# Kernel tuning notes

Measured on AMD Instinct MI355X. Metric: run time of the kernel, lower is better.

Reference implementation:

```python
import jax, jax.numpy as jnp
import numpy as np

N, E, DIN, DOUT = 50000, 625000, 128, 128


def setup_inputs() -> dict:
    key = jax.random.key(0)
    k = jax.random.split(key, 4)
    x = jax.random.normal(k[0], (N, DIN), dtype=jnp.float32)
    edge_index = jax.random.randint(k[1], (2, E), 0, N, dtype=jnp.int32)
    s = 1.0 / np.sqrt(DIN)  # Glorot-ish init like torch Linear
    W_fwd = jax.random.uniform(k[2], (DIN, DOUT), jnp.float32, -s, s)
    W_bwd = jax.random.uniform(k[3], (DIN, DOUT), jnp.float32, -s, s)
    b_fwd = jnp.zeros((DOUT,), jnp.float32)
    b_bwd = jnp.zeros((DOUT,), jnp.float32)
    return {"x": x, "edge_index": edge_index, "W_fwd": W_fwd, "b_fwd": b_fwd,
            "W_bwd": W_bwd, "b_bwd": b_bwd}


def gcn_conv(x, W, b, src, dst, n):
    """PyG GCNConv: add self-loops, symmetric degree norm, gather-scatter aggregate."""
    loops = jnp.arange(n, dtype=src.dtype)
    src2 = jnp.concatenate([src, loops])  # [E+N]
    dst2 = jnp.concatenate([dst, loops])
    ones = jnp.ones(src2.shape[0], dtype=x.dtype)
    deg = jax.ops.segment_sum(ones, dst2, num_segments=n)  # in-degree incl. self-loop
    dinv = jnp.where(deg > 0, jax.lax.rsqrt(deg), 0.0)
    norm = dinv[src2] * dinv[dst2]  # [E+N]
    h = x @ W  # [N, DOUT] dense GEMM before message passing
    msgs = h[src2] * norm[:, None]  # gather + scale, [E+N, DOUT]
    out = jax.ops.segment_sum(msgs, dst2, num_segments=n)  # scatter-add
    return out + b


def reference(x, edge_index, W_fwd, b_fwd, W_bwd, b_bwd):
    src, dst = edge_index[0], edge_index[1]
    n = x.shape[0]
    x_forward = gcn_conv(x, W_fwd, b_fwd, src, dst, n)
    # reversed edge direction for the backward diffusion conv
    x_backward = gcn_conv(x, W_bwd, b_bwd, dst, src, n)
    # dropout omitted (eval mode / deterministic reference)
    return jax.nn.relu(x_forward + x_backward)
```

## Files before the change

### kernel.cpp

```cpp
#include <hip/hip_runtime.h>
#include <hip/hip_bf16.h>
#include <cstdint>

static constexpr int BLK      = 256;
static constexpr int CAP      = 40;
static constexpr int BINSHIFT = 8;
static constexpr int BINNODES = 1 << BINSHIFT;
static constexpr int BINCAP   = BINNODES * CAP / 2;
static constexpr int EPB      = 2048;
static constexpr int OVMAX    = 1024;
static constexpr int NB2MAX   = 512;

typedef __attribute__((ext_vector_type(8))) short bf16x8;
typedef __attribute__((ext_vector_type(4))) float f32x4;

__device__ __forceinline__ float bf16lo(uint32_t u) { return __uint_as_float(u << 16); }
__device__ __forceinline__ float bf16hi(uint32_t u) { return __uint_as_float(u & 0xffff0000u); }
__device__ __forceinline__ unsigned short f2bf(float f) {
    __hip_bfloat16 h = __float2bfloat16(f);
    return *(unsigned short*)&h;
}

__global__ __launch_bounds__(BLK) void k_bin(
        const int* __restrict__ src, const int* __restrict__ dst, int ne,
        uint32_t* __restrict__ pair, int* __restrict__ gcnt,
        int* __restrict__ ovcnt, int* __restrict__ ovlist, int nbins) {
    __shared__ uint32_t stage[EPB * 2];
    __shared__ int hist[NB2MAX];
    __shared__ int lofs[NB2MAX];
    __shared__ int gbase[NB2MAX];
    __shared__ int chunk[NB2MAX / 8];
    const int tid = threadIdx.x, bid = blockIdx.x;
    const int nb2 = 2 * nbins;
    for (int i = tid; i < nb2; i += BLK) hist[i] = 0;
    __syncthreads();

    int s[8], d[8];
    const int e0 = bid * EPB + tid;
#pragma unroll
    for (int k = 0; k < 8; ++k) {
        int e = e0 + k * BLK;
        bool v = e < ne;
        s[k] = v ? src[e] : -1;
        d[k] = v ? dst[e] : -1;
        if (v) {
            atomicAdd(&hist[d[k] >> BINSHIFT], 1);
            atomicAdd(&hist[nbins + (s[k] >> BINSHIFT)], 1);
        }
    }
    __syncthreads();

    const int nch = (nb2 + 7) >> 3;
    if (tid < nch) {
        int a = 0, base = tid << 3;
#pragma unroll
        for (int k = 0; k < 8; ++k) { int idx = base + k; if (idx < nb2) a += hist[idx]; }
        chunk[tid] = a;
    }
    __syncthreads();
    if (tid == 0) { int a = 0; for (int c = 0; c < nch; ++c) { int t = chunk[c]; chunk[c] = a; a += t; } }
    __syncthreads();
    for (int i = tid; i < nb2; i += BLK) {
        int a = chunk[i >> 3];
        for (int k = (i >> 3) << 3; k < i; ++k) a += hist[k];
        lofs[i] = a;
    }
    __syncthreads();
    for (int i = tid; i < nb2; i += BLK) {
        int c = hist[i];
        gbase[i] = c ? atomicAdd(&gcnt[i], c) : 0;
        hist[i] = lofs[i];
    }
    __syncthreads();
#pragma unroll
    for (int k = 0; k < 8; ++k) {
        if (s[k] >= 0) {
            int b0 = d[k] >> BINSHIFT;
            int p0 = atomicAdd(&hist[b0], 1);
            stage[p0] = ((uint32_t)d[k] << 16) | (uint32_t)s[k];
            int b1 = nbins + (s[k] >> BINSHIFT);
            int p1 = atomicAdd(&hist[b1], 1);
            stage[p1] = ((uint32_t)s[k] << 16) | (uint32_t)d[k];
        }
    }
    __syncthreads();
    int nval = ne - bid * EPB; if (nval > EPB) nval = EPB; if (nval < 0) nval = 0;
    const int total = 2 * nval;
    for (int i = tid; i < total; i += BLK) {
        int lo = 0, hi = nb2 - 1;
        while (lo < hi) { int mid = (lo + hi + 1) >> 1; if (lofs[mid] <= i) lo = mid; else hi = mid - 1; }
        int gidx = gbase[lo] + (i - lofs[lo]);
        if (gidx < BINCAP)
            pair[(size_t)lo * BINCAP + gidx] = stage[i];
        else {
            int node = (int)(stage[i] >> 16);
            int q = atomicAdd(ovcnt, 1);
            if (q < OVMAX) ovlist[q] = (node << 1) | (lo >= nbins ? 1 : 0);
        }
    }
}

__global__ __launch_bounds__(BLK) void k_build_conv(
        uint32_t* __restrict__ pair, const int* __restrict__ gcnt,
        int* __restrict__ cnt_f, int* __restrict__ cnt_b,
        float* __restrict__ dinv_f, float* __restrict__ dinv_b,
        int* __restrict__ ovcnt, int* __restrict__ ovlist,
        const float* __restrict__ x, uint32_t* __restrict__ xb32, int nxw, int gxc,
        const float* __restrict__ Wf, const float* __restrict__ Wb,
        unsigned short* __restrict__ WTf, unsigned short* __restrict__ WTb,
        int n, int nbins) {
    const int bid = blockIdx.x, tid = threadIdx.x;
    const int nb2 = 2 * nbins;
    if (bid < nb2) {
        __shared__ unsigned short buck[BINNODES * CAP];
        __shared__ int lcnt[BINNODES];
        lcnt[tid] = 0;
        __syncthreads();
        int count = gcnt[bid]; if (count > BINCAP) count = BINCAP;
        const uint32_t* pb = pair + (size_t)bid * BINCAP;
        const int dir = bid >= nbins ? 1 : 0;
        for (int i = tid; i < count; i += BLK) {
            uint32_t p = pb[i];
            int l = (p >> 16) & (BINNODES - 1);
            int r = atomicAdd(&lcnt[l], 1);
            if (r < CAP) buck[l * CAP + r] = (unsigned short)(p & 0xffffu);
            else {
                int q = atomicAdd(ovcnt, 1);
                if (q < OVMAX)
                    ovlist[q] = (((((bid - dir * nbins) << BINSHIFT) + l)) << 1) | dir;
            }
        }
        __syncthreads();
        const int node = ((bid - dir * nbins) << BINSHIFT) + tid;
        if (node < n) {
            int c = lcnt[tid];
            if (dir) { cnt_b[node] = c; dinv_b[node] = rsqrtf(1.0f + (float)c); }
            else     { cnt_f[node] = c; dinv_f[node] = rsqrtf(1.0f + (float)c); }
        }
        uint32_t* seg = pair + (size_t)bid * BINCAP;
        const uint32_t* b32 = (const uint32_t*)buck;
        for (int i = tid; i < BINCAP; i += BLK) seg[i] = b32[i];
        return;
    }
    if (bid < nb2 + gxc) {
        int base = (bid - nb2) * 2048;
        int end = base + 2048; if (end > nxw) end = nxw;
        for (int i = base + tid; i < end; i += BLK) {
            float2 v = ((const float2*)x)[i];
            xb32[i] = ((uint32_t)f2bf(v.y) << 16) | (uint32_t)f2bf(v.x);
        }
        return;
    }
    int wb = bid - nb2 - gxc;
    for (int idx = wb * 2048 + tid; idx < (wb + 1) * 2048; idx += BLK) {
        int c = idx >> 7, k = idx & 127;
        WTf[c * 128 + k] = f2bf(Wf[k * 128 + c]);
        WTb[c * 128 + k] = f2bf(Wb[k * 128 + c]);
    }
}

__device__ __forceinline__ void accum_range(
        int j0, int j1, int ofs, float sc,
        const uint32_t* __restrict__ xb, int lane, float& a0, float& a1) {
    int j = j0;
    for (; j + 8 <= j1; j += 8) {
        int   o0 = __shfl(ofs, j + 0), o1 = __shfl(ofs, j + 1);
        int   o2 = __shfl(ofs, j + 2), o3 = __shfl(ofs, j + 3);
        int   o4 = __shfl(ofs, j + 4), o5 = __shfl(ofs, j + 5);
        int   o6 = __shfl(ofs, j + 6), o7 = __shfl(ofs, j + 7);
        float s0 = __shfl(sc, j + 0), s1 = __shfl(sc, j + 1);
        float s2 = __shfl(sc, j + 2), s3 = __shfl(sc, j + 3);
        float s4 = __shfl(sc, j + 4), s5 = __shfl(sc, j + 5);
        float s6 = __shfl(sc, j + 6), s7 = __shfl(sc, j + 7);
        uint32_t u0 = xb[(size_t)(o0 + lane)], u1 = xb[(size_t)(o1 + lane)];
        uint32_t u2 = xb[(size_t)(o2 + lane)], u3 = xb[(size_t)(o3 + lane)];
        uint32_t u4 = xb[(size_t)(o4 + lane)], u5 = xb[(size_t)(o5 + lane)];
        uint32_t u6 = xb[(size_t)(o6 + lane)], u7 = xb[(size_t)(o7 + lane)];
        a0 = fmaf(s0, bf16lo(u0), a0); a1 = fmaf(s0, bf16hi(u0), a1);
        a0 = fmaf(s1, bf16lo(u1), a0); a1 = fmaf(s1, bf16hi(u1), a1);
        a0 = fmaf(s2, bf16lo(u2), a0); a1 = fmaf(s2, bf16hi(u2), a1);
        a0 = fmaf(s3, bf16lo(u3), a0); a1 = fmaf(s3, bf16hi(u3), a1);
        a0 = fmaf(s4, bf16lo(u4), a0); a1 = fmaf(s4, bf16hi(u4), a1);
        a0 = fmaf(s5, bf16lo(u5), a0); a1 = fmaf(s5, bf16hi(u5), a1);
        a0 = fmaf(s6, bf16lo(u6), a0); a1 = fmaf(s6, bf16hi(u6), a1);
        a0 = fmaf(s7, bf16lo(u7), a0); a1 = fmaf(s7, bf16hi(u7), a1);
    }
    for (; j + 4 <= j1; j += 4) {
        int   o0 = __shfl(ofs, j + 0), o1 = __shfl(ofs, j + 1);
        int   o2 = __shfl(ofs, j + 2), o3 = __shfl(ofs, j + 3);
        float s0 = __shfl(sc, j + 0), s1 = __shfl(sc, j + 1);
        float s2 = __shfl(sc, j + 2), s3 = __shfl(sc, j + 3);
        uint32_t u0 = xb[(size_t)(o0 + lane)], u1 = xb[(size_t)(o1 + lane)];
        uint32_t u2 = xb[(size_t)(o2 + lane)], u3 = xb[(size_t)(o3 + lane)];
        a0 = fmaf(s0, bf16lo(u0), a0); a1 = fmaf(s0, bf16hi(u0), a1);
        a0 = fmaf(s1, bf16lo(u1), a0); a1 = fmaf(s1, bf16hi(u1), a1);
        a0 = fmaf(s2, bf16lo(u2), a0); a1 = fmaf(s2, bf16hi(u2), a1);
        a0 = fmaf(s3, bf16lo(u3), a0); a1 = fmaf(s3, bf16hi(u3), a1);
    }
    for (; j < j1; ++j) {
        int oj = __shfl(ofs, j); float sj = __shfl(sc, j);
        uint32_t uj = xb[(size_t)(oj + lane)];
        a0 = fmaf(sj, bf16lo(uj), a0); a1 = fmaf(sj, bf16hi(uj), a1);
    }
}

__global__ __launch_bounds__(BLK) void k_gather_agg(
        const int* __restrict__ cnt_f, const int* __restrict__ cnt_b,
        const unsigned short* __restrict__ adj_f,
        const unsigned short* __restrict__ adj_b,
        const float* __restrict__ dinv_f, const float* __restrict__ dinv_b,
        const uint32_t* __restrict__ xb32,
        uint32_t* __restrict__ agg32,
        int n, int gnode,
        const int* __restrict__ ovcnt, const int* __restrict__ ovlist,
        const int* __restrict__ src, const int* __restrict__ dst, int ne) {
    const int bid = blockIdx.x;
    if (bid < gnode) {
        const int wave = threadIdx.x >> 6;
        const int lane = threadIdx.x & 63;
        const int node = bid * 4 + wave;
        if (node >= n) return;

        int cf = cnt_f[node], cb = cnt_b[node];
        if (cf > CAP || cb > CAP) return;

        float dvsf = dinv_f[node], dvsb = dinv_b[node];
        uint32_t uv = xb32[(size_t)node * 64 + lane];
        float accf0 = dvsf * dvsf * bf16lo(uv), accf1 = dvsf * dvsf * bf16hi(uv);
        float accb0 = dvsb * dvsb * bf16lo(uv), accb1 = dvsb * dvsb * bf16hi(uv);

        const int mt = cf + cb;
        if (mt <= 64) {
            int ofs = 0; float sc = 0.f;
            if (lane < cf) {
                int nb = adj_f[node * CAP + lane];
                ofs = nb * 64;
                sc  = dvsf * dinv_f[nb];
            } else if (lane < mt) {
                int nb = adj_b[node * CAP + (lane - cf)];
                ofs = nb * 64;
                sc  = dvsb * dinv_b[nb];
            }
            accum_range(0,  cf, ofs, sc, xb32, lane, accf0, accf1);
            accum_range(cf, mt, ofs, sc, xb32, lane, accb0, accb1);
        } else {
            for (int j = 0; j < cf; ++j) {
                int nb = adj_f[node * CAP + j];
                float dj = dvsf * dinv_f[nb];
                uint32_t u = xb32[(size_t)nb * 64 + lane];
                accf0 = fmaf(dj, bf16lo(u), accf0); accf1 = fmaf(dj, bf16hi(u), accf1);
            }
            for (int j = 0; j < cb; ++j) {
                int nb = adj_b[node * CAP + j];
                float dj = dvsb * dinv_b[nb];
                uint32_t u = xb32[(size_t)nb * 64 + lane];
                accb0 = fmaf(dj, bf16lo(u), accb0); accb1 = fmaf(dj, bf16hi(u), accb1);
            }
        }
        agg32[(size_t)node * 128 + lane] =
            ((uint32_t)f2bf(accf1) << 16) | (uint32_t)f2bf(accf0);
        agg32[(size_t)node * 128 + 64 + lane] =
            ((uint32_t)f2bf(accb1) << 16) | (uint32_t)f2bf(accb0);
        return;
    }

    int nov = *ovcnt; if (nov > OVMAX) nov = OVMAX;
    if (nov == 0) return;
    __shared__ int lst[4096];
    __shared__ int lc;
    const int tid = threadIdx.x;
    for (int i = bid - gnode; i < nov; i += 8) {
        int node = ovlist[i] >> 1;
        for (int d2 = 0; d2 < 2; ++d2) {
            const int* key = d2 ? src : dst;
            const int* val = d2 ? dst : src;
            const float* dinv = d2 ? dinv_b : dinv_f;
            float dvs = dinv[node];
            float s0 = 0.f, s1 = 0.f;
            if (tid < 64) {
                uint32_t u = xb32[(size_t)node * 64 + tid];
                s0 = dvs * bf16lo(u); s1 = dvs * bf16hi(u);
            }
            for (int start = 0; start < ne; start += 4096) {
                if (tid == 0) lc = 0;
                __syncthreads();
                int end = min(start + 4096, ne);
                for (int e2 = start + tid; e2 < end; e2 += BLK)
                    if (key[e2] == node) { int q = atomicAdd(&lc, 1); lst[q] = val[e2]; }
                __syncthreads();
                int mm = lc;
                if (tid < 64) {
                    for (int j = 0; j < mm; ++j) {
                        int nb = lst[j];
                        float dv = dinv[nb];
                        uint32_t u = xb32[(size_t)nb * 64 + tid];
                        s0 = fmaf(dv, bf16lo(u), s0);
                        s1 = fmaf(dv, bf16hi(u), s1);
                    }
                }
                __syncthreads();
            }
            if (tid < 64) {
                float a0 = dvs * s0, a1 = dvs * s1;
                agg32[(size_t)node * 128 + d2 * 64 + tid] =
                    ((uint32_t)f2bf(a1) << 16) | (uint32_t)f2bf(a0);
            }
            __syncthreads();
        }
    }
}

__global__ __launch_bounds__(BLK) void k_gemm_out(
        const unsigned short* __restrict__ agg,
        const unsigned short* __restrict__ WTf,
        const unsigned short* __restrict__ WTb,
        const float* __restrict__ bfv, const float* __restrict__ bbv,
        float* __restrict__ out, int n) {
    const int wave = threadIdx.x >> 6, lane = threadIdx.x & 63;
    const int wm = wave >> 1, wh = wave & 1;
    const int q = lane >> 4, t16 = lane & 15;
    const int m0 = blockIdx.x * 32 + wm * 16;
    int arow = m0 + t16; if (arow >= n) arow = n - 1;
    const unsigned short* ra = agg + (size_t)arow * 256;
    bf16x8 af[4], ab[4];
#pragma unroll
    for (int s = 0; s < 4; ++s) {
        af[s] = *(const bf16x8*)(ra + s * 32 + q * 8);
        ab[s] = *(const bf16x8*)(ra + 128 + s * 32 + q * 8);
    }
    __syncthreads();
#pragma unroll
    for (int t = 0; t < 4; ++t) {
        const int col = wh * 64 + t * 16 + t16;
        const unsigned short* wrf = WTf + (size_t)col * 128;
        const unsigned short* wrb = WTb + (size_t)col * 128;
        f32x4 c = {0.f, 0.f, 0.f, 0.f};
#pragma unroll
        for (int s = 0; s < 4; ++s)
            c = __builtin_amdgcn_mfma_f32_16x16x32_bf16(
                    af[s], *(const bf16x8*)(wrf + s * 32 + q * 8), c, 0, 0, 0);
#pragma unroll
        for (int s = 0; s < 4; ++s)
            c = __builtin_amdgcn_mfma_f32_16x16x32_bf16(
                    ab[s], *(const bf16x8*)(wrb + s * 32 + q * 8), c, 0, 0, 0);
        const float bias = bfv[col] + bbv[col];
#pragma unroll
        for (int r = 0; r < 4; ++r) {
            int row = m0 + q * 4 + r;
            if (row < n)
                out[(size_t)row * 128 + col] = fmaxf(c[r] + bias, 0.f);
        }
    }
}

extern "C" void kernel_launch(void* const* d_in, const int* in_sizes, int n_in,
                              void* d_out, int out_size, void* d_ws, size_t ws_size,
                              hipStream_t stream) {
    const float* x  = (const float*)d_in[0];
    const int*   ei = (const int*)d_in[1];
    const float* Wf = (const float*)d_in[2];
    const float* bf = (const float*)d_in[3];
    const float* Wb = (const float*)d_in[4];
    const float* bb = (const float*)d_in[5];

    const int n  = in_sizes[0] / 128;
    const int ne = in_sizes[1] / 2;
    const int* src = ei;
    const int* dst = ei + ne;
    float* out = (float*)d_out;

    const int nbins = (n + BINNODES - 1) >> BINSHIFT;
    const int nb2   = 2 * nbins;

    char* w = (char*)d_ws;
    uint32_t* pair = (uint32_t*)w;              w += (size_t)nb2 * BINCAP * 4;
    uint32_t* xb32 = (uint32_t*)w;              w += (size_t)n * 64 * 4;
    float* dinv_f = (float*)w;                  w += (size_t)n * 4;
    float* dinv_b = (float*)w;                  w += (size_t)n * 4;
    unsigned short* WTf = (unsigned short*)w;   w += 128 * 128 * 2;
    unsigned short* WTb = (unsigned short*)w;   w += 128 * 128 * 2;
    int* cnt_f = (int*)w;                       w += (size_t)n * 4;
    int* cnt_b = (int*)w;                       w += (size_t)n * 4;
    int* gcnt = (int*)w;                        w += (size_t)nb2 * 4;
    int* ovcnt = (int*)w;                       w += 8 * 4;
    int* ovlist = (int*)w;                      w += OVMAX * 4;

    const unsigned short* adj_f = (const unsigned short*)pair;
    const unsigned short* adj_b = adj_f + (size_t)nbins * BINNODES * CAP;
    uint32_t* agg32 = (uint32_t*)d_out;

    const int gbin  = (ne + EPB - 1) / EPB;
    const int gxc   = (n * 64 + 2047) / 2048;
    const int gnode = (n + 3) / 4;
    const int ggo   = (n + 31) / 32;

    hipMemsetAsync(gcnt, 0, (size_t)(nb2 + 8) * 4, stream);

    k_bin<<<gbin, BLK, 0, stream>>>(src, dst, ne, pair, gcnt, ovcnt, ovlist, nbins);

    k_build_conv<<<nb2 + gxc + 8, BLK, 0, stream>>>(pair, gcnt,
                                                    cnt_f, cnt_b, dinv_f, dinv_b,
                                                    ovcnt, ovlist,
                                                    x, xb32, n * 64, gxc,
                                                    Wf, Wb, WTf, WTb, n, nbins);

    k_gather_agg<<<gnode + 8, BLK, 0, stream>>>(cnt_f, cnt_b, adj_f, adj_b,
                                                dinv_f, dinv_b, xb32,
                                                agg32, n, gnode,
                                                ovcnt, ovlist, src, dst, ne);

    k_gemm_out<<<ggo, BLK, 0, stream>>>((const unsigned short*)agg32,
                                        WTf, WTb, bf, bb, out, n);
}
```

Measured before the change: 199.4 us.

## Fuse all phases into one persistent cooperative kernel with grid syncs

Replaces the memset and four separate kernel launches with a single cooperative persistent kernel. Its five phases (weight and x conversion, edge binning, bucket build, gather-aggregate, MFMA GEMM) are separated by grid-wide syncs and use grid-stride loops. It also halves edges per binning block and records each staged entry's bin index, so the per-element binary search is no longer needed. The aim is to remove launch gaps and the memset. In exchange, occupancy is capped by the cooperative grid size, and grid syncs plus grid-stride loops add overhead to the memory-bound gather phase.

After: 597.6 us. 3x slower.

```diff
diff --git a/kernel.cpp b/kernel.cpp
--- a/kernel.cpp
+++ b/kernel.cpp
@@ -1,15 +1,18 @@
 #include <hip/hip_runtime.h>
 #include <hip/hip_bf16.h>
+#include <hip/hip_cooperative_groups.h>
 #include <cstdint>
 
-static constexpr int BLK      = 256;
+namespace cg = cooperative_groups;
+
 static constexpr int CAP      = 40;
 static constexpr int BINSHIFT = 8;
 static constexpr int BINNODES = 1 << BINSHIFT;
 static constexpr int BINCAP   = BINNODES * CAP / 2;
-static constexpr int EPB      = 2048;
+static constexpr int EPB      = 1024;
 static constexpr int OVMAX    = 1024;
 static constexpr int NB2MAX   = 512;
+static constexpr int SMEM_SZ  = 21504;
 
 typedef __attribute__((ext_vector_type(8))) short bf16x8;
 typedef __attribute__((ext_vector_type(4))) float f32x4;
@@ -21,145 +24,157 @@
     return *(unsigned short*)&h;
 }
 
-__global__ __launch_bounds__(BLK) void k_bin(
-        const int* __restrict__ src, const int* __restrict__ dst, int ne,
-        uint32_t* __restrict__ pair, int* __restrict__ gcnt,
-        int* __restrict__ ovcnt, int* __restrict__ ovlist, int nbins) {
-    __shared__ uint32_t stage[EPB * 2];
-    __shared__ int hist[NB2MAX];
-    __shared__ int lofs[NB2MAX];
-    __shared__ int gbase[NB2MAX];
-    __shared__ int chunk[NB2MAX / 8];
-    const int tid = threadIdx.x, bid = blockIdx.x;
-    const int nb2 = 2 * nbins;
-    for (int i = tid; i < nb2; i += BLK) hist[i] = 0;
-    __syncthreads();
-
-    int s[8], d[8];
-    const int e0 = bid * EPB + tid;
-#pragma unroll
-    for (int k = 0; k < 8; ++k) {
-        int e = e0 + k * BLK;
-        bool v = e < ne;
-        s[k] = v ? src[e] : -1;
-        d[k] = v ? dst[e] : -1;
-        if (v) {
-            atomicAdd(&hist[d[k] >> BINSHIFT], 1);
-            atomicAdd(&hist[nbins + (s[k] >> BINSHIFT)], 1);
-        }
-    }
-    __syncthreads();
-
-    const int nch = (nb2 + 7) >> 3;
-    if (tid < nch) {
-        int a = 0, base = tid << 3;
-#pragma unroll
-        for (int k = 0; k < 8; ++k) { int idx = base + k; if (idx < nb2) a += hist[idx]; }
-        chunk[tid] = a;
-    }
-    __syncthreads();
-    if (tid == 0) { int a = 0; for (int c = 0; c < nch; ++c) { int t = chunk[c]; chunk[c] = a; a += t; } }
-    __syncthreads();
-    for (int i = tid; i < nb2; i += BLK) {
-        int a = chunk[i >> 3];
-        for (int k = (i >> 3) << 3; k < i; ++k) a += hist[k];
-        lofs[i] = a;
-    }
-    __syncthreads();
-    for (int i = tid; i < nb2; i += BLK) {
-        int c = hist[i];
-        gbase[i] = c ? atomicAdd(&gcnt[i], c) : 0;
-        hist[i] = lofs[i];
-    }
-    __syncthreads();
-#pragma unroll
-    for (int k = 0; k < 8; ++k) {
-        if (s[k] >= 0) {
-            int b0 = d[k] >> BINSHIFT;
-            int p0 = atomicAdd(&hist[b0], 1);
-            stage[p0] = ((uint32_t)d[k] << 16) | (uint32_t)s[k];
-            int b1 = nbins + (s[k] >> BINSHIFT);
-            int p1 = atomicAdd(&hist[b1], 1);
-            stage[p1] = ((uint32_t)s[k] << 16) | (uint32_t)d[k];
-        }
-    }
-    __syncthreads();
-    int nval = ne - bid * EPB; if (nval > EPB) nval = EPB; if (nval < 0) nval = 0;
-    const int total = 2 * nval;
-    for (int i = tid; i < total; i += BLK) {
-        int lo = 0, hi = nb2 - 1;
-        while (lo < hi) { int mid = (lo + hi + 1) >> 1; if (lofs[mid] <= i) lo = mid; else hi = mid - 1; }
-        int gidx = gbase[lo] + (i - lofs[lo]);
-        if (gidx < BINCAP)
-            pair[(size_t)lo * BINCAP + gidx] = stage[i];
-        else {
-            int node = (int)(stage[i] >> 16);
-            int q = atomicAdd(ovcnt, 1);
-            if (q < OVMAX) ovlist[q] = (node << 1) | (lo >= nbins ? 1 : 0);
-        }
-    }
-}
-
-__global__ __launch_bounds__(BLK) void k_build_conv(
-        uint32_t* __restrict__ pair, const int* __restrict__ gcnt,
-        int* __restrict__ cnt_f, int* __restrict__ cnt_b,
-        float* __restrict__ dinv_f, float* __restrict__ dinv_b,
-        int* __restrict__ ovcnt, int* __restrict__ ovlist,
-        const float* __restrict__ x, uint32_t* __restrict__ xb32, int nxw, int gxc,
-        const float* __restrict__ Wf, const float* __restrict__ Wb,
-        unsigned short* __restrict__ WTf, unsigned short* __restrict__ WTb,
-        int n, int nbins) {
-    const int bid = blockIdx.x, tid = threadIdx.x;
-    const int nb2 = 2 * nbins;
-    if (bid < nb2) {
-        __shared__ unsigned short buck[BINNODES * CAP];
-        __shared__ int lcnt[BINNODES];
+struct P {
+    const int* src; const int* dst; int ne;
+    uint32_t* pair; int* gcnt; int* ovcnt; int* ovlist;
+    int nbins, nb2, gbin, gxc, ggo, n;
+    const float* x; uint32_t* xb32; int nxw;
+    const float* Wf; const float* Wb;
+    unsigned short* WTf; unsigned short* WTb;
+    int* cnt_f; int* cnt_b; float* dinv_f; float* dinv_b;
+    const unsigned short* adj_f; const unsigned short* adj_b;
+    const float* bfv; const float* bbv;
+    float* out;
+};
+
+__device__ void phaseA(const P& A) {
+    const int G = gridDim.x, tid = threadIdx.x;
+    const int ta = 9 + A.gxc;
+    for (int t = blockIdx.x; t < ta; t += G) {
+        if (t < 8) {
+            for (int idx = t * 2048 + tid; idx < (t + 1) * 2048; idx += 256) {
+                int c = idx >> 7, k = idx & 127;
+                A.WTf[c * 128 + k] = f2bf(A.Wf[k * 128 + c]);
+                A.WTb[c * 128 + k] = f2bf(A.Wb[k * 128 + c]);
+            }
+        } else if (t == 8) {
+            for (int i = tid; i < A.nb2 + 8; i += 256) A.gcnt[i] = 0;
+        } else {
+            int base = (t - 9) * 2048;
+            int end = base + 2048; if (end > A.nxw) end = A.nxw;
+            for (int i = base + tid; i < end; i += 256) {
+                float2 v = ((const float2*)A.x)[i];
+                A.xb32[i] = ((uint32_t)f2bf(v.y) << 16) | (uint32_t)f2bf(v.x);
+            }
+        }
+    }
+}
+
+__device__ void phaseB(const P& A, char* smem) {
+    uint32_t*       stage = (uint32_t*)smem;
+    unsigned short* binof = (unsigned short*)(smem + 8192);
+    int*            hist  = (int*)(smem + 12288);
+    int*            lofs  = (int*)(smem + 14336);
+    int*            gbase = (int*)(smem + 16384);
+    int*            chunk = (int*)(smem + 18432);
+    const int G = gridDim.x, tid = threadIdx.x;
+    const int nb2 = A.nb2;
+    for (int t = blockIdx.x; t < A.gbin; t += G) {
+        for (int i = tid; i < nb2; i += 256) hist[i] = 0;
+        __syncthreads();
+        int s[4], d[4];
+        const int e0 = t * EPB + tid;
+#pragma unroll
+        for (int k = 0; k < 4; ++k) {
+            int e = e0 + k * 256;
+            bool v = e < A.ne;
+            s[k] = v ? A.src[e] : -1;
+            d[k] = v ? A.dst[e] : -1;
+            if (v) {
+                atomicAdd(&hist[d[k] >> BINSHIFT], 1);
+                atomicAdd(&hist[A.nbins + (s[k] >> BINSHIFT)], 1);
+            }
+        }
+        __syncthreads();
+        const int nch = (nb2 + 7) >> 3;
+        if (tid < nch) {
+            int a = 0, base = tid << 3;
+#pragma unroll
+            for (int k = 0; k < 8; ++k) { int idx = base + k; if (idx < nb2) a += hist[idx]; }
+            chunk[tid] = a;
+        }
+        __syncthreads();
+        if (tid == 0) { int a = 0; for (int c = 0; c < nch; ++c) { int tt = chunk[c]; chunk[c] = a; a += tt; } }
+        __syncthreads();
+        for (int i = tid; i < nb2; i += 256) {
+            int a = chunk[i >> 3];
+            for (int k = (i >> 3) << 3; k < i; ++k) a += hist[k];
+            lofs[i] = a;
+        }
+        __syncthreads();
+        for (int i = tid; i < nb2; i += 256) {
+            int c = hist[i];
+            gbase[i] = c ? atomicAdd(&A.gcnt[i], c) : 0;
+            hist[i] = lofs[i];
+        }
+        __syncthreads();
+#pragma unroll
+        for (int k = 0; k < 4; ++k) {
+            if (s[k] >= 0) {
+                int b0 = d[k] >> BINSHIFT;
+                int p0 = atomicAdd(&hist[b0], 1);
+                stage[p0] = ((uint32_t)d[k] << 16) | (uint32_t)s[k];
+                binof[p0] = (unsigned short)b0;
+                int b1 = A.nbins + (s[k] >> BINSHIFT);
+                int p1 = atomicAdd(&hist[b1], 1);
+                stage[p1] = ((uint32_t)s[k] << 16) | (uint32_t)d[k];
+                binof[p1] = (unsigned short)b1;
+            }
+        }
+        __syncthreads();
+        int nval = A.ne - t * EPB; if (nval > EPB) nval = EPB; if (nval < 0) nval = 0;
+        const int total = 2 * nval;
+        for (int i = tid; i < total; i += 256) {
+            int b = binof[i];
+            int gidx = gbase[b] + (i - lofs[b]);
+            if (gidx < BINCAP)
+                A.pair[(size_t)b * BINCAP + gidx] = stage[i];
+            else {
+                int node = (int)(stage[i] >> 16);
+                int q = atomicAdd(A.ovcnt, 1);
+                if (q < OVMAX) A.ovlist[q] = (node << 1) | (b >= A.nbins ? 1 : 0);
+            }
+        }
+        __syncthreads();
+    }
+}
+
+__device__ void phaseC(const P& A, char* smem) {
+    unsigned short* buck = (unsigned short*)smem;
+    int*            lcnt = (int*)(smem + 20480);
+    const int tid = threadIdx.x;
+    for (int b = blockIdx.x; b < A.nb2; b += gridDim.x) {
         lcnt[tid] = 0;
         __syncthreads();
-        int count = gcnt[bid]; if (count > BINCAP) count = BINCAP;
-        const uint32_t* pb = pair + (size_t)bid * BINCAP;
-        const int dir = bid >= nbins ? 1 : 0;
-        for (int i = tid; i < count; i += BLK) {
+        int count = A.gcnt[b]; if (count > BINCAP) count = BINCAP;
+        const uint32_t* pb = A.pair + (size_t)b * BINCAP;
+        const int dir = b >= A.nbins ? 1 : 0;
+        for (int i = tid; i < count; i += 256) {
             uint32_t p = pb[i];
             int l = (p >> 16) & (BINNODES - 1);
             int r = atomicAdd(&lcnt[l], 1);
             if (r < CAP) buck[l * CAP + r] = (unsigned short)(p & 0xffffu);
             else {
-                int q = atomicAdd(ovcnt, 1);
+                int q = atomicAdd(A.ovcnt, 1);
                 if (q < OVMAX)
-                    ovlist[q] = (((((bid - dir * nbins) << BINSHIFT) + l)) << 1) | dir;
-            }
-        }
-        __syncthreads();
-        const int node = ((bid - dir * nbins) << BINSHIFT) + tid;
-        if (node < n) {
+                    A.ovlist[q] = (((((b - dir * A.nbins) << BINSHIFT) + l)) << 1) | dir;
+            }
+        }
+        __syncthreads();
+        const int node = ((b - dir * A.nbins) << BINSHIFT) + tid;
+        if (node < A.n) {
             int c = lcnt[tid];
-            if (dir) { cnt_b[node] = c; dinv_b[node] = rsqrtf(1.0f + (float)c); }
-            else     { cnt_f[node] = c; dinv_f[node] = rsqrtf(1.0f + (float)c); }
-        }
-        uint32_t* seg = pair + (size_t)bid * BINCAP;
+            if (dir) { A.cnt_b[node] = c; A.dinv_b[node] = rsqrtf(1.0f + (float)c); }
+            else     { A.cnt_f[node] = c; A.dinv_f[node] = rsqrtf(1.0f + (float)c); }
+        }
+        uint32_t* seg = A.pair + (size_t)b * BINCAP;
         const uint32_t* b32 = (const uint32_t*)buck;
-        for (int i = tid; i < BINCAP; i += BLK) seg[i] = b32[i];
-        return;
-    }
-    if (bid < nb2 + gxc) {
-        int base = (bid - nb2) * 2048;
-        int end = base + 2048; if (end > nxw) end = nxw;
-        for (int i = base + tid; i < end; i += BLK) {
-            float2 v = ((const float2*)x)[i];
-            xb32[i] = ((uint32_t)f2bf(v.y) << 16) | (uint32_t)f2bf(v.x);
-        }
-        return;
-    }
-    int wb = bid - nb2 - gxc;
-    for (int idx = wb * 2048 + tid; idx < (wb + 1) * 2048; idx += BLK) {
-        int c = idx >> 7, k = idx & 127;
-        WTf[c * 128 + k] = f2bf(Wf[k * 128 + c]);
-        WTb[c * 128 + k] = f2bf(Wb[k * 128 + c]);
-    }
-}
-
-__device__ __forceinline__ void accum_range(
+        for (int i = tid; i < BINCAP; i += 256) seg[i] = b32[i];
+        __syncthreads();
+    }
+}
+
+__device__ void accum_range(
         int j0, int j1, int ofs, float sc,
         const uint32_t* __restrict__ xb, int lane, float& a0, float& a1) {
     int j = j0;
@@ -204,28 +219,18 @@
     }
 }
 
-__global__ __launch_bounds__(BLK) void k_gather_agg(
-        const int* __restrict__ cnt_f, const int* __restrict__ cnt_b,
-        const unsigned short* __restrict__ adj_f,
-        const unsigned short* __restrict__ adj_b,
-        const float* __restrict__ dinv_f, const float* __restrict__ dinv_b,
-        const uint32_t* __restrict__ xb32,
-        uint32_t* __restrict__ agg32,
-        int n, int gnode,
-        const int* __restrict__ ovcnt, const int* __restrict__ ovlist,
-        const int* __restrict__ src, const int* __restrict__ dst, int ne) {
-    const int bid = blockIdx.x;
-    if (bid < gnode) {
-        const int wave = threadIdx.x >> 6;
-        const int lane = threadIdx.x & 63;
-        const int node = bid * 4 + wave;
-        if (node >= n) return;
-
-        int cf = cnt_f[node], cb = cnt_b[node];
-        if (cf > CAP || cb > CAP) return;
-
-        float dvsf = dinv_f[node], dvsb = dinv_b[node];
-        uint32_t uv = xb32[(size_t)node * 64 + lane];
+__device__ void phaseD(const P& A, char* smem) {
+    const int tid = threadIdx.x;
+    const int wv = tid >> 6, lane = tid & 63;
+    const int NW = gridDim.x * 4;
+    uint32_t* agg32 = (uint32_t*)A.out;
+
+    for (int node = blockIdx.x * 4 + wv; node < A.n; node += NW) {
+        int cf = A.cnt_f[node], cb = A.cnt_b[node];
+        if (cf > CAP || cb > CAP) continue;
+
+        float dvsf = A.dinv_f[node], dvsb = A.dinv_b[node];
+        uint32_t uv = A.xb32[(size_t)node * 64 + lane];
         float accf0 = dvsf * dvsf * bf16lo(uv), accf1 = dvsf * dvsf * bf16hi(uv);
         float accb0 = dvsb * dvsb * bf16lo(uv), accb1 = dvsb * dvsb * bf16hi(uv);
 
@@ -233,27 +238,27 @@
         if (mt <= 64) {
             int ofs = 0; float sc = 0.f;
             if (lane < cf) {
-                int nb = adj_f[node * CAP + lane];
+                int nb = A.adj_f[node * CAP + lane];
                 ofs = nb * 64;
-                sc  = dvsf * dinv_f[nb];
+                sc  = dvsf * A.dinv_f[nb];
             } else if (lane < mt) {
-                int nb = adj_b[node * CAP + (lane - cf)];
+                int nb = A.adj_b[node * CAP + (lane - cf)];
                 ofs = nb * 64;
-                sc  = dvsb * dinv_b[nb];
-            }
-            accum_range(0,  cf, ofs, sc, xb32, lane, accf0, accf1);
-            accum_range(cf, mt, ofs, sc, xb32, lane, accb0, accb1);
+                sc  = dvsb * A.dinv_b[nb];
+            }
+            accum_range(0,  cf, ofs, sc, A.xb32, lane, accf0, accf1);
+            accum_range(cf, mt, ofs, sc, A.xb32, lane, accb0, accb1);
         } else {
             for (int j = 0; j < cf; ++j) {
-                int nb = adj_f[node * CAP + j];
-                float dj = dvsf * dinv_f[nb];
-                uint32_t u = xb32[(size_t)nb * 64 + lane];
+                int nb = A.adj_f[node * CAP + j];
+                float dj = dvsf * A.dinv_f[nb];
+                uint32_t u = A.xb32[(size_t)nb * 64 + lane];
                 accf0 = fmaf(dj, bf16lo(u), accf0); accf1 = fmaf(dj, bf16hi(u), accf1);
             }
             for (int j = 0; j < cb; ++j) {
-                int nb = adj_b[node * CAP + j];
-                float dj = dvsb * dinv_b[nb];
-                uint32_t u = xb32[(size_t)nb * 64 + lane];
+                int nb = A.adj_b[node * CAP + j];
+                float dj = dvsb * A.dinv_b[nb];
+                uint32_t u = A.xb32[(size_t)nb * 64 + lane];
                 accb0 = fmaf(dj, bf16lo(u), accb0); accb1 = fmaf(dj, bf16hi(u), accb1);
             }
         }
@@ -261,97 +266,119 @@
             ((uint32_t)f2bf(accf1) << 16) | (uint32_t)f2bf(accf0);
         agg32[(size_t)node * 128 + 64 + lane] =
             ((uint32_t)f2bf(accb1) << 16) | (uint32_t)f2bf(accb0);
-        return;
-    }
-
-    int nov = *ovcnt; if (nov > OVMAX) nov = OVMAX;
-    if (nov == 0) return;
-    __shared__ int lst[4096];
-    __shared__ int lc;
-    const int tid = threadIdx.x;
-    for (int i = bid - gnode; i < nov; i += 8) {
-        int node = ovlist[i] >> 1;
-        for (int d2 = 0; d2 < 2; ++d2) {
-            const int* key = d2 ? src : dst;
-            const int* val = d2 ? dst : src;
-            const float* dinv = d2 ? dinv_b : dinv_f;
-            float dvs = dinv[node];
-            float s0 = 0.f, s1 = 0.f;
-            if (tid < 64) {
-                uint32_t u = xb32[(size_t)node * 64 + tid];
-                s0 = dvs * bf16lo(u); s1 = dvs * bf16hi(u);
-            }
-            for (int start = 0; start < ne; start += 4096) {
-                if (tid == 0) lc = 0;
-                __syncthreads();
-                int end = min(start + 4096, ne);
-                for (int e2 = start + tid; e2 < end; e2 += BLK)
-                    if (key[e2] == node) { int q = atomicAdd(&lc, 1); lst[q] = val[e2]; }
-                __syncthreads();
-                int mm = lc;
+    }
+
+    if (blockIdx.x < 8) {
+        __syncthreads();
+        int nov = *A.ovcnt; if (nov > OVMAX) nov = OVMAX;
+        if (nov == 0) return;
+        int* lst = (int*)smem;
+        int* lcp = (int*)(smem + 8192);
+        for (int i = blockIdx.x; i < nov; i += 8) {
+            int node = A.ovlist[i] >> 1;
+            for (int d2 = 0; d2 < 2; ++d2) {
+                const int* key = d2 ? A.src : A.dst;
+                const int* val = d2 ? A.dst : A.src;
+                const float* dinv = d2 ? A.dinv_b : A.dinv_f;
+                float dvs = dinv[node];
+                float s0 = 0.f, s1 = 0.f;
                 if (tid < 64) {
-                    for (int j = 0; j < mm; ++j) {
-                        int nb = lst[j];
-                        float dv = dinv[nb];
-                        uint32_t u = xb32[(size_t)nb * 64 + tid];
-                        s0 = fmaf(dv, bf16lo(u), s0);
-                        s1 = fmaf(dv, bf16hi(u), s1);
+                    uint32_t u = A.xb32[(size_t)node * 64 + tid];
+                    s0 = dvs * bf16lo(u); s1 = dvs * bf16hi(u);
+                }
+                for (int start = 0; start < A.ne; start += 2048) {
+                    if (tid == 0) *lcp = 0;
+                    __syncthreads();
+                    int end = min(start + 2048, A.ne);
+                    for (int e2 = start + tid; e2 < end; e2 += 256)
+                        if (key[e2] == node) { int q = atomicAdd(lcp, 1); lst[q] = val[e2]; }
+                    __syncthreads();
+                    int mm = *lcp;
+                    if (tid < 64) {
+                        for (int j = 0; j < mm; ++j) {
+                            int nb = lst[j];
+                            float dv = dinv[nb];
+                            uint32_t u = A.xb32[(size_t)nb * 64 + tid];
+                            s0 = fmaf(dv, bf16lo(u), s0);
+                            s1 = fmaf(dv, bf16hi(u), s1);
+                        }
                     }
+                    __syncthreads();
+                }
+                if (tid < 64) {
+                    float a0 = dvs * s0, a1 = dvs * s1;
+                    agg32[(size_t)node * 128 + d2 * 64 + tid] =
+                        ((uint32_t)f2bf(a1) << 16) | (uint32_t)f2bf(a0);
                 }
                 __syncthreads();
             }
-            if (tid < 64) {
-                float a0 = dvs * s0, a1 = dvs * s1;
-                agg32[(size_t)node * 128 + d2 * 64 + tid] =
-                    ((uint32_t)f2bf(a1) << 16) | (uint32_t)f2bf(a0);
-            }
-            __syncthreads();
-        }
-    }
-}
-
-__global__ __launch_bounds__(BLK) void k_gemm_out(
-        const unsigned short* __restrict__ agg,
-        const unsigned short* __restrict__ WTf,
-        const unsigned short* __restrict__ WTb,
-        const float* __restrict__ bfv, const float* __restrict__ bbv,
-        float* __restrict__ out, int n) {
-    const int wave = threadIdx.x >> 6, lane = threadIdx.x & 63;
+        }
+    }
+}
+
+__device__ void phaseE(const P& A) {
+    const int tid = threadIdx.x;
+    const int wave = tid >> 6, lane = tid & 63;
     const int wm = wave >> 1, wh = wave & 1;
     const int q = lane >> 4, t16 = lane & 15;
-    const int m0 = blockIdx.x * 32 + wm * 16;
-    int arow = m0 + t16; if (arow >= n) arow = n - 1;
-    const unsigned short* ra = agg + (size_t)arow * 256;
-    bf16x8 af[4], ab[4];
-#pragma unroll
-    for (int s = 0; s < 4; ++s) {
-        af[s] = *(const bf16x8*)(ra + s * 32 + q * 8);
-        ab[s] = *(const bf16x8*)(ra + 128 + s * 32 + q * 8);
-    }
-    __syncthreads();
-#pragma unroll
-    for (int t = 0; t < 4; ++t) {
-        const int col = wh * 64 + t * 16 + t16;
-        const unsigned short* wrf = WTf + (size_t)col * 128;
-        const unsigned short* wrb = WTb + (size_t)col * 128;
-        f32x4 c = {0.f, 0.f, 0.f, 0.f};
-#pragma unroll
-        for (int s = 0; s < 4; ++s)
-            c = __builtin_amdgcn_mfma_f32_16x16x32_bf16(
-                    af[s], *(const bf16x8*)(wrf + s * 32 + q * 8), c, 0, 0, 0);
-#pragma unroll
-        for (int s = 0; s < 4; ++s)
-            c = __builtin_amdgcn_mfma_f32_16x16x32_bf16(
-                    ab[s], *(const bf16x8*)(wrb + s * 32 + q * 8), c, 0, 0, 0);
-        const float bias = bfv[col] + bbv[col];
-#pragma unroll
-        for (int r = 0; r < 4; ++r) {
-            int row = m0 + q * 4 + r;
-            if (row < n)
-                out[(size_t)row * 128 + col] = fmaxf(c[r] + bias, 0.f);
-        }
-    }
-}
+    const unsigned short* agg = (const unsigned short*)A.out;
+    for (int t = blockIdx.x; t < A.ggo; t += gridDim.x) {
+        const int m0 = t * 32 + wm * 16;
+        int arow = m0 + t16; if (arow >= A.n) arow = A.n - 1;
+        const unsigned short* ra = agg + (size_t)arow * 256;
+        bf16x8 af[4], ab[4];
+#pragma unroll
+        for (int s = 0; s < 4; ++s) {
+            af[s] = *(const bf16x8*)(ra + s * 32 + q * 8);
+            ab[s] = *(const bf16x8*)(ra + 128 + s * 32 + q * 8);
+        }
+        __syncthreads();
+#pragma unroll
+        for (int t4 = 0; t4 < 4; ++t4) {
+            const int col = wh * 64 + t4 * 16 + t16;
+            const unsigned short* wrf = A.WTf + (size_t)col * 128;
+            const unsigned short* wrb = A.WTb + (size_t)col * 128;
+            f32x4 c = {0.f, 0.f, 0.f, 0.f};
+#pragma unroll
+            for (int s = 0; s < 4; ++s)
+                c = __builtin_amdgcn_mfma_f32_16x16x32_bf16(
+                        af[s], *(const bf16x8*)(wrf + s * 32 + q * 8), c, 0, 0, 0);
+#pragma unroll
+            for (int s = 0; s < 4; ++s)
+                c = __builtin_amdgcn_mfma_f32_16x16x32_bf16(
+                        ab[s], *(const bf16x8*)(wrb + s * 32 + q * 8), c, 0, 0, 0);
+            const float bias = A.bfv[col] + A.bbv[col];
+#pragma unroll
+            for (int r = 0; r < 4; ++r) {
+                int row = m0 + q * 4 + r;
+                if (row < A.n)
+                    A.out[(size_t)row * 128 + col] = fmaxf(c[r] + bias, 0.f);
+            }
+        }
+    }
+}
+
+__global__ __launch_bounds__(256, 6) void k_mega(P A) {
+    __shared__ __align__(16) char smem[SMEM_SZ];
+    cg::grid_group g = cg::this_grid();
+    phaseA(A);        g.sync();
+    phaseB(A, smem);  g.sync();
+    phaseC(A, smem);  g.sync();
+    phaseD(A, smem);  g.sync();
+    phaseE(A);
+}
+
+__global__ __launch_bounds__(256) void k_pA(P A) { phaseA(A); }
+__global__ __launch_bounds__(256) void k_pB(P A) {
+    __shared__ __align__(16) char smem[SMEM_SZ]; phaseB(A, smem);
+}
+__global__ __launch_bounds__(256) void k_pC(P A) {
+    __shared__ __align__(16) char smem[SMEM_SZ]; phaseC(A, smem);
+}
+__global__ __launch_bounds__(256) void k_pD(P A) {
+    __shared__ __align__(16) char smem[SMEM_SZ]; phaseD(A, smem);
+}
+__global__ __launch_bounds__(256) void k_pE(P A) { phaseE(A); }
 
 extern "C" void kernel_launch(void* const* d_in, const int* in_sizes, int n_in,
                               void* d_out, int out_size, void* d_ws, size_t ws_size,
@@ -365,10 +392,6 @@
 
     const int n  = in_sizes[0] / 128;
     const int ne = in_sizes[1] / 2;
-    const int* src = ei;
-    const int* dst = ei + ne;
-    float* out = (float*)d_out;
-
     const int nbins = (n + BINNODES - 1) >> BINSHIFT;
     const int nb2   = 2 * nbins;
 
@@ -385,30 +408,36 @@
     int* ovcnt = (int*)w;                       w += 8 * 4;
     int* ovlist = (int*)w;                      w += OVMAX * 4;
 
-    const unsigned short* adj_f = (const unsigned short*)pair;
-    const unsigned short* adj_b = adj_f + (size_t)nbins * BINNODES * CAP;
-    uint32_t* agg32 = (uint32_t*)d_out;
-
-    const int gbin  = (ne + EPB - 1) / EPB;
-    const int gxc   = (n * 64 + 2047) / 2048;
-    const int gnode = (n + 3) / 4;
-    const int ggo   = (n + 31) / 32;
-
-    hipMemsetAsync(gcnt, 0, (size_t)(nb2 + 8) * 4, stream);
-
-    k_bin<<<gbin, BLK, 0, stream>>>(src, dst, ne, pair, gcnt, ovcnt, ovlist, nbins);
-
-    k_build_conv<<<nb2 + gxc + 8, BLK, 0, stream>>>(pair, gcnt,
-                                                    cnt_f, cnt_b, dinv_f, dinv_b,
-                                                    ovcnt, ovlist,
-                                                    x, xb32, n * 64, gxc,
-                                                    Wf, Wb, WTf, WTb, n, nbins);
-
-    k_gather_agg<<<gnode + 8, BLK, 0, stream>>>(cnt_f, cnt_b, adj_f, adj_b,
-                                                dinv_f, dinv_b, xb32,
-                                                agg32, n, gnode,
-                                                ovcnt, ovlist, src, dst, ne);
-
-    k_gemm_out<<<ggo, BLK, 0, stream>>>((const unsigned short*)agg32,
-                                        WTf, WTb, bf, bb, out, n);
-}
+    P a;
+    a.src = ei; a.dst = ei + ne; a.ne = ne;
+    a.pair = pair; a.gcnt = gcnt; a.ovcnt = ovcnt; a.ovlist = ovlist;
+    a.nbins = nbins; a.nb2 = nb2;
+    a.gbin = (ne + EPB - 1) / EPB;
+    a.gxc  = (n * 64 + 2047) / 2048;
+    a.ggo  = (n + 31) / 32;
+    a.n = n;
+    a.x = x; a.xb32 = xb32; a.nxw = n * 64;
+    a.Wf = Wf; a.Wb = Wb; a.WTf = WTf; a.WTb = WTb;
+    a.cnt_f = cnt_f; a.cnt_b = cnt_b; a.dinv_f = dinv_f; a.dinv_b = dinv_b;
+    a.adj_f = (const unsigned short*)pair;
+    a.adj_b = (const unsigned short*)pair + (size_t)nbins * BINNODES * CAP;
+    a.bfv = bf; a.bbv = bb;
+    a.out = (float*)d_out;
+
+    int nbmax = 0;
+    hipError_t err = hipOccupancyMaxActiveBlocksPerMultiprocessor(&nbmax, k_mega, 256, 0);
+    bool launched = false;
+    if (err == hipSuccess && nbmax > 0) {
+        int grid = nbmax * 256;
+        void* ka[] = { (void*)&a };
+        err = hipLaunchCooperativeKernel(k_mega, dim3(grid), dim3(256), ka, 0, stream);
+        launched = (err == hipSuccess);
+    }
+    if (!launched) {
+        k_pA<<<9 + a.gxc, 256, 0, stream>>>(a);
+        k_pB<<<a.gbin,    256, 0, stream>>>(a);
+        k_pC<<<a.nb2,     256, 0, stream>>>(a);
+        k_pD<<<(n + 3)/4, 256, 0, stream>>>(a);
+        k_pE<<<a.ggo,     256, 0, stream>>>(a);
+    }
+}
```
